# Optimization experiments

Hardware: AMD Instinct MI355X
Metric: run time of the kernel (lower is better)

Reference implementation:

```python
import jax, jax.numpy as jnp
import numpy as np

N_NODES = 20000
N_EDGES = 320000
NUM_GRAPHS = 64
IN_DIM = 256


def setup_inputs() -> dict:
    key = jax.random.key(0)
    ks = jax.random.split(key, 12)
    x = jax.random.normal(ks[0], (N_NODES, IN_DIM), dtype=jnp.float32)
    edge_index = jax.random.randint(ks[1], (2, N_EDGES), 0, N_NODES, dtype=jnp.int64)
    batch = jnp.sort(jax.random.randint(ks[2], (N_NODES,), 0, NUM_GRAPHS, dtype=jnp.int64))
    def glorot(k, shape):
        lim = float(np.sqrt(6.0 / (shape[0] + shape[1])))
        return jax.random.uniform(k, shape, dtype=jnp.float32, minval=-lim, maxval=lim)
    W1 = glorot(ks[3], (IN_DIM, 256)); b1 = jnp.zeros((256,), jnp.float32)
    W2 = glorot(ks[4], (256, 128));   b2 = jnp.zeros((128,), jnp.float32)
    Wl1 = glorot(ks[5], (128, 64));   bl1 = jnp.zeros((64,), jnp.float32)
    Wl2 = glorot(ks[6], (64, 1));     bl2 = jnp.zeros((1,), jnp.float32)
    return {"x": x, "edge_index": edge_index, "batch": batch,
            "W1": W1, "b1": b1, "W2": W2, "b2": b2,
            "Wl1": Wl1, "bl1": bl1, "Wl2": Wl2, "bl2": bl2}


def gcn_conv(x, src, dst, W, b, n_nodes):
    # PyG GCNConv: add self-loops, symmetric normalization D^-1/2 (A+I) D^-1/2,
    # linear transform first, then gather-scale-scatter aggregation, then bias.
    loop = jnp.arange(n_nodes, dtype=src.dtype)
    s = jnp.concatenate([src, loop])
    d = jnp.concatenate([dst, loop])
    deg = jax.ops.segment_sum(jnp.ones_like(d, dtype=x.dtype), d, num_segments=n_nodes)
    dinv = jnp.where(deg > 0, jax.lax.rsqrt(deg), 0.0)
    norm = dinv[s] * dinv[d]                         # [E+N]
    h = x @ W                                        # [N, out]
    msg = h[s] * norm[:, None]                       # [E+N, out]
    out = jax.ops.segment_sum(msg, d, num_segments=n_nodes)
    return out + b


def global_mean_pool(x, batch, num_graphs):
    sums = jax.ops.segment_sum(x, batch, num_segments=num_graphs)
    cnts = jax.ops.segment_sum(jnp.ones((x.shape[0],), x.dtype), batch, num_segments=num_graphs)
    return sums / jnp.maximum(cnts, 1.0)[:, None]


def reference(x, edge_index, batch, W1, b1, W2, b2, Wl1, bl1, Wl2, bl2):
    n = x.shape[0]
    src, dst = edge_index[0], edge_index[1]
    h = jax.nn.relu(gcn_conv(x, src, dst, W1, b1, n))   # dropout = identity (eval)
    h = jax.nn.relu(gcn_conv(h, src, dst, W2, b2, n))
    g = global_mean_pool(h, batch, NUM_GRAPHS)          # [G, 128]
    g = jax.nn.relu(g @ Wl1 + bl1)
    return jax.nn.sigmoid(g @ Wl2 + bl2)                # [G, 1]
```

## Files before the change

### kernel.cpp

```cpp
#include <hip/hip_runtime.h>
#include <hip/hip_bf16.h>
#include <math.h>

typedef __attribute__((ext_vector_type(8))) short bf16x8;
typedef __attribute__((ext_vector_type(4))) float f32x4;
typedef __attribute__((ext_vector_type(2))) float f32x2;

__device__ __forceinline__ unsigned short f2bf(float f) {
    unsigned int u = __float_as_uint(f);
    unsigned int r = (u + 0x7FFFu + ((u >> 16) & 1u)) >> 16;
    return (unsigned short)r;
}
__device__ __forceinline__ unsigned int pk2bf(float lo, float hi) {
    unsigned int r;
    asm("v_cvt_pk_bf16_f32 %0, %1, %2" : "=v"(r) : "v"(lo), "v"(hi));
    return r;
}
__device__ __forceinline__ unsigned char f2fp8(float v) {
    int p = __builtin_amdgcn_cvt_pk_fp8_f32(v, v, 0, false);
    return (unsigned char)(p & 0xff);
}
__device__ __forceinline__ unsigned int pk4fp8(float a, float b, float c, float d) {
    int p = __builtin_amdgcn_cvt_pk_fp8_f32(a, b, 0, false);
    p = __builtin_amdgcn_cvt_pk_fp8_f32(c, d, p, true);
    return (unsigned int)p;
}
#if __has_builtin(__builtin_amdgcn_cvt_pk_f32_fp8)
__device__ __forceinline__ void fp8x8_add(uint2 u, float* a) {
    f32x2 p0 = __builtin_amdgcn_cvt_pk_f32_fp8((int)u.x, false);
    f32x2 p1 = __builtin_amdgcn_cvt_pk_f32_fp8((int)u.x, true);
    f32x2 p2 = __builtin_amdgcn_cvt_pk_f32_fp8((int)u.y, false);
    f32x2 p3 = __builtin_amdgcn_cvt_pk_f32_fp8((int)u.y, true);
    a[0] += p0.x; a[1] += p0.y; a[2] += p1.x; a[3] += p1.y;
    a[4] += p2.x; a[5] += p2.y; a[6] += p3.x; a[7] += p3.y;
}
__device__ __forceinline__ void fp8x4_add(unsigned int u, float* a) {
    f32x2 p0 = __builtin_amdgcn_cvt_pk_f32_fp8((int)u, false);
    f32x2 p1 = __builtin_amdgcn_cvt_pk_f32_fp8((int)u, true);
    a[0] += p0.x; a[1] += p0.y; a[2] += p1.x; a[3] += p1.y;
}
#else
__device__ __forceinline__ void fp8x8_add(uint2 u, float* a) {
    a[0] += __builtin_amdgcn_cvt_f32_fp8((int)u.x, 0);
    a[1] += __builtin_amdgcn_cvt_f32_fp8((int)u.x, 1);
    a[2] += __builtin_amdgcn_cvt_f32_fp8((int)u.x, 2);
    a[3] += __builtin_amdgcn_cvt_f32_fp8((int)u.x, 3);
    a[4] += __builtin_amdgcn_cvt_f32_fp8((int)u.y, 0);
    a[5] += __builtin_amdgcn_cvt_f32_fp8((int)u.y, 1);
    a[6] += __builtin_amdgcn_cvt_f32_fp8((int)u.y, 2);
    a[7] += __builtin_amdgcn_cvt_f32_fp8((int)u.y, 3);
}
__device__ __forceinline__ void fp8x4_add(unsigned int u, float* a) {
    a[0] += __builtin_amdgcn_cvt_f32_fp8((int)u, 0);
    a[1] += __builtin_amdgcn_cvt_f32_fp8((int)u, 1);
    a[2] += __builtin_amdgcn_cvt_f32_fp8((int)u, 2);
    a[3] += __builtin_amdgcn_cvt_f32_fp8((int)u, 3);
}
#endif
__device__ __forceinline__ float deg_dinv(int c) { return rsqrtf((float)c + 1.0f); }

__device__ __forceinline__ void load_lds16(const unsigned short* g, unsigned short* l) {
    __builtin_amdgcn_global_load_lds(
        (const __attribute__((address_space(1))) unsigned int*)g,
        (__attribute__((address_space(3))) unsigned int*)l, 16, 0, 0);
}
__device__ __forceinline__ void load_lds16_u8(const unsigned char* g, unsigned char* l) {
    __builtin_amdgcn_global_load_lds(
        (const __attribute__((address_space(1))) unsigned int*)g,
        (__attribute__((address_space(3))) unsigned int*)l, 16, 0, 0);
}

__global__ __launch_bounds__(256) void prepfill_kernel(const int* __restrict__ src,
                                                       const int* __restrict__ dst,
                                                       int* __restrict__ cnt,
                                                       int* __restrict__ csr,
                                                       const int* __restrict__ batch,
                                                       int* __restrict__ gstart,
                                                       const float* __restrict__ W1,
                                                       unsigned short* __restrict__ w1t,
                                                       const float* __restrict__ W2,
                                                       unsigned char* __restrict__ w2t8,
                                                       int N, int G, int E, int FB, int CWB) {
    int b = blockIdx.x;
    int tid = threadIdx.x;
    if (b < FB) {
        int e = (b * 256 + tid) * 4;
        if (e + 3 < E) {
            int4 d4 = *(const int4*)(dst + e);
            int4 s4 = *(const int4*)(src + e);
            int sl;
            sl = atomicAdd(&cnt[d4.x], 1); if (sl < 64) csr[(d4.x << 6) + sl] = s4.x;
            sl = atomicAdd(&cnt[d4.y], 1); if (sl < 64) csr[(d4.y << 6) + sl] = s4.y;
            sl = atomicAdd(&cnt[d4.z], 1); if (sl < 64) csr[(d4.z << 6) + sl] = s4.z;
            sl = atomicAdd(&cnt[d4.w], 1); if (sl < 64) csr[(d4.w << 6) + sl] = s4.w;
        } else {
            for (; e < E; e++) {
                int d = dst[e];
                int slot = atomicAdd(&cnt[d], 1);
                if (slot < 64) csr[(d << 6) + slot] = src[e];
            }
        }
        return;
    }
    b -= FB;
    if (b < CWB) {
        int idx = b * 256 + tid;
        if (idx < 256 * 256) {
            int m = idx >> 8, k = idx & 255;
            w1t[idx] = f2bf(W1[(size_t)k * 256 + m]);
        } else if (idx < 256 * 256 + 128 * 256) {
            int j = idx - 256 * 256;
            int m = j >> 8, k = j & 255;
            w2t8[j] = f2fp8(W2[(size_t)k * 128 + m]);
        }
        return;
    }
    b -= CWB;
    {
        int i = b * 256 + tid;
        if (i >= N) return;
        int bb = batch[i];
        if (i == 0) { for (int g = 0; g <= bb; g++) gstart[g] = 0; }
        else { int bp = batch[i - 1]; for (int g = bp + 1; g <= bb; g++) gstart[g] = i; }
        if (i == N - 1) { for (int g = bb + 1; g <= G; g++) gstart[g] = N; }
    }
}

__global__ __launch_bounds__(256) void gemm1_kernel(const float* __restrict__ x,
                                                    const unsigned short* __restrict__ Bt,
                                                    const int* __restrict__ cnt,
                                                    unsigned char* __restrict__ C8, int N) {
    __shared__ unsigned short As[128 * 32];
    __shared__ unsigned short Bs[128 * 32];
    int gb = blockIdx.x;
    int bx = gb & 1, by = gb >> 1;
    const int K = 256;
    int tid = threadIdx.x;
    int wave = tid >> 6, lane = tid & 63;
    int quad = lane >> 4, m16 = lane & 15;
    int r0 = by * 128, c0 = bx * 128;
    int srow = lane >> 2;
    int skoff = (lane & 3) * 8;

    f32x4 acc[2][8];
#pragma unroll
    for (int rg = 0; rg < 2; rg++)
#pragma unroll
        for (int ct = 0; ct < 8; ct++) acc[rg][ct] = (f32x4){0.f, 0.f, 0.f, 0.f};

    int arow = tid >> 1, akh = tid & 1;
    int agrow = r0 + arow; if (agrow >= N) agrow = N - 1;
    const float* ap = x + (size_t)agrow * K + akh * 16;
    int asw = (arow >> 1) & 3;
    unsigned short* as0 = As + arow * 32 + ((((akh << 1) | 0) ^ asw) << 3);
    unsigned short* as1 = As + arow * 32 + ((((akh << 1) | 1) ^ asw) << 3);
    int rsw = (m16 >> 1) & 3;

    for (int kb = 0; kb < K; kb += 32) {
        float4 f0 = *(const float4*)(ap + kb);
        float4 f1 = *(const float4*)(ap + kb + 4);
        float4 f2 = *(const float4*)(ap + kb + 8);
        float4 f3 = *(const float4*)(ap + kb + 12);
        {
            int bcol = wave * 16 + srow;
            load_lds16(Bt + (size_t)(c0 + bcol) * K + kb + skoff, Bs + (wave * 16) * 32);
            load_lds16(Bt + (size_t)(c0 + 64 + bcol) * K + kb + skoff, Bs + (64 + wave * 16) * 32);
        }
        uint4 u0, u1;
        u0.x = pk2bf(f0.x, f0.y); u0.y = pk2bf(f0.z, f0.w);
        u0.z = pk2bf(f1.x, f1.y); u0.w = pk2bf(f1.z, f1.w);
        u1.x = pk2bf(f2.x, f2.y); u1.y = pk2bf(f2.z, f2.w);
        u1.z = pk2bf(f3.x, f3.y); u1.w = pk2bf(f3.z, f3.w);
        *(uint4*)as0 = u0;
        *(uint4*)as1 = u1;
        __syncthreads();
        bf16x8 af[2], bfr[8];
#pragma unroll
        for (int rg = 0; rg < 2; rg++)
            af[rg] = *(const bf16x8*)(As + (wave * 32 + rg * 16 + m16) * 32 + ((quad ^ rsw) << 3));
#pragma unroll
        for (int ct = 0; ct < 8; ct++)
            bfr[ct] = *(const bf16x8*)(Bs + (ct * 16 + m16) * 32 + (quad << 3));
#pragma unroll
        for (int rg = 0; rg < 2; rg++)
#pragma unroll
            for (int ct = 0; ct < 8; ct++)
                acc[rg][ct] = __builtin_amdgcn_mfma_f32_16x16x32_bf16(af[rg], bfr[ct], acc[rg][ct], 0, 0, 0);
        __syncthreads();
    }
    float di[2][4];
#pragma unroll
    for (int rg = 0; rg < 2; rg++)
#pragma unroll
        for (int r = 0; r < 4; r++) {
            int row = r0 + wave * 32 + rg * 16 + quad * 4 + r;
            di[rg][r] = (row < N) ? deg_dinv(cnt[row]) : 1.f;
        }
#pragma unroll
    for (int rg = 0; rg < 2; rg++) {
#pragma unroll
        for (int ct = 0; ct < 8; ct++) {
            int col = c0 + ct * 16 + m16;
#pragma unroll
            for (int r = 0; r < 4; r++) {
                int row = r0 + wave * 32 + rg * 16 + quad * 4 + r;
                if (row < N) C8[(size_t)row * 256 + col] = f2fp8(acc[rg][ct][r] * di[rg][r]);
            }
        }
    }
}

__global__ __launch_bounds__(256) void gemm2_kernel(const unsigned char* __restrict__ A,
                                                    const unsigned char* __restrict__ Bt,
                                                    const int* __restrict__ cnt,
                                                    unsigned char* __restrict__ C8, int N) {
    __shared__ unsigned char As8[128 * 32];
    __shared__ unsigned char Bs8[64 * 32];
    const int K = 256;
    int tid = threadIdx.x;
    int wave = tid >> 6, lane = tid & 63;
    int quad = lane >> 4, m16 = lane & 15;
    int bx = blockIdx.x, by = blockIdx.y;
    int r0 = by * 128, c0 = bx * 64;

    f32x4 acc[2][4];
#pragma unroll
    for (int rg = 0; rg < 2; rg++)
#pragma unroll
        for (int ct = 0; ct < 4; ct++) acc[rg][ct] = (f32x4){0.f, 0.f, 0.f, 0.f};

    int arow = wave * 32 + (lane >> 1);
    int agrow = r0 + arow; if (agrow >= N) agrow = N - 1;
    int ach = (lane & 1) * 16;
    int brow = (wave & 1) * 32 + (lane >> 1);
    int bch = (lane & 1) * 16;

    for (int kb = 0; kb < K; kb += 32) {
        load_lds16_u8(A + (size_t)agrow * K + kb + ach, As8 + (wave * 32) * 32);
        if (wave < 2)
            load_lds16_u8(Bt + (size_t)(c0 + brow) * K + kb + bch, Bs8 + (wave * 32) * 32);
        __syncthreads();
        long af[2], bfr[4];
#pragma unroll
        for (int rg = 0; rg < 2; rg++)
            af[rg] = *(const long*)(As8 + (wave * 32 + rg * 16 + m16) * 32 + (quad << 3));
#pragma unroll
        for (int ct = 0; ct < 4; ct++)
            bfr[ct] = *(const long*)(Bs8 + (ct * 16 + m16) * 32 + (quad << 3));
#pragma unroll
        for (int rg = 0; rg < 2; rg++)
#pragma unroll
            for (int ct = 0; ct < 4; ct++)
                acc[rg][ct] = __builtin_amdgcn_mfma_f32_16x16x32_fp8_fp8(af[rg], bfr[ct], acc[rg][ct], 0, 0, 0);
        __syncthreads();
    }
    float di[2][4];
#pragma unroll
    for (int rg = 0; rg < 2; rg++)
#pragma unroll
        for (int r = 0; r < 4; r++) {
            int row = r0 + wave * 32 + rg * 16 + quad * 4 + r;
            di[rg][r] = (row < N) ? deg_dinv(cnt[row]) : 1.f;
        }
#pragma unroll
    for (int rg = 0; rg < 2; rg++) {
#pragma unroll
        for (int ct = 0; ct < 4; ct++) {
            int col = c0 + ct * 16 + m16;
#pragma unroll
            for (int r = 0; r < 4; r++) {
                int row = r0 + wave * 32 + rg * 16 + quad * 4 + r;
                if (row < N) C8[(size_t)row * 128 + col] = f2fp8(acc[rg][ct][r] * di[rg][r]);
            }
        }
    }
}

__global__ __launch_bounds__(256) void gather256_kernel(const unsigned char* __restrict__ h8,
                                                        const int* __restrict__ csr,
                                                        const int* __restrict__ cnt,
                                                        const float* __restrict__ bias,
                                                        unsigned char* __restrict__ o18, int N) {
    int node = blockIdx.x * 4 + (threadIdx.x >> 6);
    if (node >= N) return;
    int lane = threadIdx.x & 63;
    int half = lane >> 5, hl = lane & 31;
    int beg = node << 6;
    int c = cnt[node];
    float dd = deg_dinv(c);
    if (c > 64) c = 64;
    int end = beg + c;
    uint2 uh = *(const uint2*)(h8 + (size_t)node * 256 + hl * 8);
    float a[8] = {0, 0, 0, 0, 0, 0, 0, 0};
    int j = beg;
    for (; j + 15 < end; j += 16) {
        int s0 = csr[j + half],      s1 = csr[j + 2 + half];
        int s2 = csr[j + 4 + half],  s3 = csr[j + 6 + half];
        int s4 = csr[j + 8 + half],  s5 = csr[j + 10 + half];
        int s6 = csr[j + 12 + half], s7 = csr[j + 14 + half];
        uint2 u0 = *(const uint2*)(h8 + (size_t)s0 * 256 + hl * 8);
        uint2 u1 = *(const uint2*)(h8 + (size_t)s1 * 256 + hl * 8);
        uint2 u2 = *(const uint2*)(h8 + (size_t)s2 * 256 + hl * 8);
        uint2 u3 = *(const uint2*)(h8 + (size_t)s3 * 256 + hl * 8);
        uint2 u4 = *(const uint2*)(h8 + (size_t)s4 * 256 + hl * 8);
        uint2 u5 = *(const uint2*)(h8 + (size_t)s5 * 256 + hl * 8);
        uint2 u6 = *(const uint2*)(h8 + (size_t)s6 * 256 + hl * 8);
        uint2 u7 = *(const uint2*)(h8 + (size_t)s7 * 256 + hl * 8);
        fp8x8_add(u0, a); fp8x8_add(u1, a); fp8x8_add(u2, a); fp8x8_add(u3, a);
        fp8x8_add(u4, a); fp8x8_add(u5, a); fp8x8_add(u6, a); fp8x8_add(u7, a);
    }
    for (; j + 7 < end; j += 8) {
        int s0 = csr[j + half], s1 = csr[j + 2 + half];
        int s2 = csr[j + 4 + half], s3 = csr[j + 6 + half];
        uint2 u0 = *(const uint2*)(h8 + (size_t)s0 * 256 + hl * 8);
        uint2 u1 = *(const uint2*)(h8 + (size_t)s1 * 256 + hl * 8);
        uint2 u2 = *(const uint2*)(h8 + (size_t)s2 * 256 + hl * 8);
        uint2 u3 = *(const uint2*)(h8 + (size_t)s3 * 256 + hl * 8);
        fp8x8_add(u0, a); fp8x8_add(u1, a); fp8x8_add(u2, a); fp8x8_add(u3, a);
    }
    for (; j + 1 < end; j += 2) {
        int s0 = csr[j + half];
        uint2 u0 = *(const uint2*)(h8 + (size_t)s0 * 256 + hl * 8);
        fp8x8_add(u0, a);
    }
    if (j < end && half == 0) {
        int s0 = csr[j];
        uint2 u0 = *(const uint2*)(h8 + (size_t)s0 * 256 + hl * 8);
        fp8x8_add(u0, a);
    }
#pragma unroll
    for (int i = 0; i < 8; i++) a[i] += __shfl_down(a[i], 32);
    if (half == 0) {
        float self[8] = {0, 0, 0, 0, 0, 0, 0, 0};
        fp8x8_add(uh, self);
        float4 bv0 = ((const float4*)bias)[hl * 2];
        float4 bv1 = ((const float4*)bias)[hl * 2 + 1];
        float bvf[8] = {bv0.x, bv0.y, bv0.z, bv0.w, bv1.x, bv1.y, bv1.z, bv1.w};
        float v[8];
#pragma unroll
        for (int i = 0; i < 8; i++) v[i] = fmaxf((a[i] + self[i]) * dd + bvf[i], 0.f);
        uint2 o;
        o.x = pk4fp8(v[0], v[1], v[2], v[3]);
        o.y = pk4fp8(v[4], v[5], v[6], v[7]);
        ((uint2*)(o18 + (size_t)node * 256))[hl] = o;
    }
}

__global__ __launch_bounds__(256) void gather128_kernel(const unsigned char* __restrict__ t8,
                                                        const int* __restrict__ csr,
                                                        const int* __restrict__ cnt,
                                                        const float* __restrict__ bias,
                                                        unsigned char* __restrict__ out2, int N) {
    int node = blockIdx.x * 4 + (threadIdx.x >> 6);
    if (node >= N) return;
    int lane = threadIdx.x & 63;
    int half = lane >> 5, hl = lane & 31;
    int beg = node << 6;
    int c = cnt[node];
    float dd = deg_dinv(c);
    if (c > 64) c = 64;
    int end = beg + c;
    unsigned int uh = *(const unsigned int*)(t8 + (size_t)node * 128 + hl * 4);
    float a[4] = {0, 0, 0, 0};
    int j = beg;
    for (; j + 15 < end; j += 16) {
        int s0 = csr[j + half],      s1 = csr[j + 2 + half];
        int s2 = csr[j + 4 + half],  s3 = csr[j + 6 + half];
        int s4 = csr[j + 8 + half],  s5 = csr[j + 10 + half];
        int s6 = csr[j + 12 + half], s7 = csr[j + 14 + half];
        unsigned int u0 = *(const unsigned int*)(t8 + (size_t)s0 * 128 + hl * 4);
        unsigned int u1 = *(const unsigned int*)(t8 + (size_t)s1 * 128 + hl * 4);
        unsigned int u2 = *(const unsigned int*)(t8 + (size_t)s2 * 128 + hl * 4);
        unsigned int u3 = *(const unsigned int*)(t8 + (size_t)s3 * 128 + hl * 4);
        unsigned int u4 = *(const unsigned int*)(t8 + (size_t)s4 * 128 + hl * 4);
        unsigned int u5 = *(const unsigned int*)(t8 + (size_t)s5 * 128 + hl * 4);
        unsigned int u6 = *(const unsigned int*)(t8 + (size_t)s6 * 128 + hl * 4);
        unsigned int u7 = *(const unsigned int*)(t8 + (size_t)s7 * 128 + hl * 4);
        fp8x4_add(u0, a); fp8x4_add(u1, a); fp8x4_add(u2, a); fp8x4_add(u3, a);
        fp8x4_add(u4, a); fp8x4_add(u5, a); fp8x4_add(u6, a); fp8x4_add(u7, a);
    }
    for (; j + 7 < end; j += 8) {
        int s0 = csr[j + half], s1 = csr[j + 2 + half];
        int s2 = csr[j + 4 + half], s3 = csr[j + 6 + half];
        unsigned int u0 = *(const unsigned int*)(t8 + (size_t)s0 * 128 + hl * 4);
        unsigned int u1 = *(const unsigned int*)(t8 + (size_t)s1 * 128 + hl * 4);
        unsigned int u2 = *(const unsigned int*)(t8 + (size_t)s2 * 128 + hl * 4);
        unsigned int u3 = *(const unsigned int*)(t8 + (size_t)s3 * 128 + hl * 4);
        fp8x4_add(u0, a); fp8x4_add(u1, a); fp8x4_add(u2, a); fp8x4_add(u3, a);
    }
    for (; j + 1 < end; j += 2) {
        int s0 = csr[j + half];
        unsigned int u0 = *(const unsigned int*)(t8 + (size_t)s0 * 128 + hl * 4);
        fp8x4_add(u0, a);
    }
    if (j < end && half == 0) {
        int s0 = csr[j];
        unsigned int u0 = *(const unsigned int*)(t8 + (size_t)s0 * 128 + hl * 4);
        fp8x4_add(u0, a);
    }
#pragma unroll
    for (int i = 0; i < 4; i++) a[i] += __shfl_down(a[i], 32);
    if (half == 0) {
        float self[4] = {0, 0, 0, 0};
        fp8x4_add(uh, self);
        float4 bv = ((const float4*)bias)[hl];
        float r0 = fmaxf((a[0] + self[0]) * dd + bv.x, 0.f);
        float r1 = fmaxf((a[1] + self[1]) * dd + bv.y, 0.f);
        float r2 = fmaxf((a[2] + self[2]) * dd + bv.z, 0.f);
        float r3 = fmaxf((a[3] + self[3]) * dd + bv.w, 0.f);
        ((unsigned int*)(out2 + (size_t)node * 128))[hl] = pk4fp8(r0, r1, r2, r3);
    }
}

__global__ __launch_bounds__(256) void poolhead_kernel(const unsigned char* __restrict__ out2,
                                                       const int* __restrict__ gstart,
                                                       float* __restrict__ gsum,
                                                       int* __restrict__ gdone,
                                                       const float* __restrict__ Wl1,
                                                       const float* __restrict__ bl1,
                                                       const float* __restrict__ Wl2,
                                                       const float* __restrict__ bl2,
                                                       float* __restrict__ out) {
    int g = blockIdx.x >> 3, slice = blockIdx.x & 7;
    int tid = threadIdx.x;
    int hw = tid >> 5, hl = tid & 31;
    int gs = gstart[g], ge = gstart[g + 1];
    float a[4] = {0, 0, 0, 0};
    for (int i = gs + slice * 8 + hw; i < ge; i += 64) {
        unsigned int u = ((const unsigned int*)(out2 + (size_t)i * 128))[hl];
        fp8x4_add(u, a);
    }
    __shared__ float red[8][128];
#pragma unroll
    for (int k = 0; k < 4; k++) red[hw][hl * 4 + k] = a[k];
    __syncthreads();
    if (tid < 128) {
        float s = 0.f;
#pragma unroll
        for (int w = 0; w < 8; w++) s += red[w][tid];
        if (s != 0.f) atomicAdd(&gsum[g * 128 + tid], s);
    }
    __syncthreads();
    __shared__ int lastflag;
    if (tid == 0) {
        __threadfence();
        int old = atomicAdd(&gdone[g], 1);
        lastflag = (old == 7) ? 1 : 0;
    }
    __syncthreads();
    if (!lastflag) return;
    __shared__ float gv[128];
    if (tid < 128) {
        float s = atomicAdd(&gsum[g * 128 + tid], 0.0f);
        float cntf = fmaxf((float)(ge - gs), 1.0f);
        gv[tid] = s / cntf;
    }
    __syncthreads();
    if (tid < 64) {
        float acc = bl1[tid];
#pragma unroll 8
        for (int k = 0; k < 128; k++) acc += gv[k] * Wl1[k * 64 + tid];
        acc = fmaxf(acc, 0.f);
        float p = acc * Wl2[tid];
#pragma unroll
        for (int off = 32; off; off >>= 1) p += __shfl_down(p, off);
        if (tid == 0) out[g] = 1.f / (1.f + expf(-(p + bl2[0])));
    }
}

extern "C" void kernel_launch(void* const* d_in, const int* in_sizes, int n_in,
                              void* d_out, int out_size, void* d_ws, size_t ws_size,
                              hipStream_t stream) {
    const float* x   = (const float*)d_in[0];
    const int* ei    = (const int*)d_in[1];
    const int* batch = (const int*)d_in[2];
    const float* W1  = (const float*)d_in[3];
    const float* b1  = (const float*)d_in[4];
    const float* W2  = (const float*)d_in[5];
    const float* b2  = (const float*)d_in[6];
    const float* Wl1 = (const float*)d_in[7];
    const float* bl1 = (const float*)d_in[8];
    const float* Wl2 = (const float*)d_in[9];
    const float* bl2 = (const float*)d_in[10];
    float* out = (float*)d_out;

    const int N = in_sizes[2];
    const int E = in_sizes[1] / 2;
    const int G = 64;
    const int* src = ei;
    const int* dst = ei + E;

    char* base = (char*)d_ws;
    size_t off = 0;
    auto carve = [&](size_t bytes) -> char* {
        char* p = base + off;
        off = (off + bytes + 15) & ~(size_t)15;
        return p;
    };
    int*   cnt    = (int*)carve((size_t)N * 4);
    float* gsum   = (float*)carve((size_t)G * 128 * 4);
    int*   gdone  = (int*)carve((size_t)G * 4);
    size_t zero_bytes = (size_t)(N + G * 128 + G) * 4 + 32;
    int*   csr    = (int*)carve((size_t)N * 64 * 4);
    int*   gstart = (int*)carve((size_t)(G + 1) * 4);
    unsigned short* w1t  = (unsigned short*)carve((size_t)256 * 256 * 2);
    unsigned char*  w2t8 = (unsigned char*)carve((size_t)128 * 256);
    unsigned char*  h8   = (unsigned char*)carve((size_t)N * 256);
    unsigned char*  o18  = (unsigned char*)carve((size_t)N * 256);
    unsigned char*  t8   = h8;
    unsigned char*  out2 = o18;

    hipMemsetAsync(d_ws, 0, zero_bytes, stream);

    const int BNB = (N + 255) / 256;
    const int CWB = (256 * 256 + 128 * 256 + 255) / 256;
    const int FB  = (E / 4 + 255) / 256;
    prepfill_kernel<<<FB + CWB + BNB, 256, 0, stream>>>(src, dst, cnt, csr, batch, gstart,
                                                        W1, w1t, W2, w2t8, N, G, E, FB, CWB);

    const int GB1 = 2 * ((N + 127) / 128);
    gemm1_kernel<<<GB1, 256, 0, stream>>>(x, w1t, cnt, h8, N);

    gather256_kernel<<<(N + 3) / 4, 256, 0, stream>>>(h8, csr, cnt, b1, o18, N);

    {
        dim3 grid(2, (N + 127) / 128);
        gemm2_kernel<<<grid, 256, 0, stream>>>(o18, w2t8, cnt, t8, N);
    }
    gather128_kernel<<<(N + 3) / 4, 256, 0, stream>>>(t8, csr, cnt, b2, out2, N);

    poolhead_kernel<<<G * 8, 256, 0, stream>>>(out2, gstart, gsum, gdone,
                                               Wl1, bl1, Wl2, bl2, out);
}
```

Baseline: 173.1 us.

## Fuse layer-1 neighbor aggregation into GEMM2 via LDS-resident tiles

```diff
diff --git a/kernel.cpp b/kernel.cpp
--- a/kernel.cpp
+++ b/kernel.cpp
@@ -210,139 +210,128 @@
     }
 }
 
-__global__ __launch_bounds__(256) void gemm2_kernel(const unsigned char* __restrict__ A,
-                                                    const unsigned char* __restrict__ Bt,
-                                                    const int* __restrict__ cnt,
-                                                    unsigned char* __restrict__ C8, int N) {
-    __shared__ unsigned char As8[128 * 32];
-    __shared__ unsigned char Bs8[64 * 32];
-    const int K = 256;
+__global__ __launch_bounds__(512) void l1agg_gemm2_kernel(const unsigned char* __restrict__ h8,
+                                                          const int* __restrict__ csr,
+                                                          const int* __restrict__ cnt,
+                                                          const float* __restrict__ b1,
+                                                          const unsigned char* __restrict__ w2t8,
+                                                          unsigned char* __restrict__ t8,
+                                                          int N) {
+    __shared__ unsigned char As8[64 * 256];
+    __shared__ unsigned char Bs8[128 * 256];
     int tid = threadIdx.x;
     int wave = tid >> 6, lane = tid & 63;
+    int r0 = blockIdx.x * 64;
+
+#pragma unroll
+    for (int q = 0; q < 4; q++) {
+        int s = q * 512 + wave * 64 + lane;
+        int r = s >> 4, sr = s & 15;
+        int gs = sr ^ (r & 7);
+        load_lds16_u8(w2t8 + (size_t)r * 256 + gs * 16,
+                      Bs8 + ((size_t)q * 512 + wave * 64) * 16);
+    }
+
+    int half_id = tid >> 5, hl = tid & 31;
+    float4 bv0 = ((const float4*)b1)[hl * 2];
+    float4 bv1 = ((const float4*)b1)[hl * 2 + 1];
+    float bvf[8] = {bv0.x, bv0.y, bv0.z, bv0.w, bv1.x, bv1.y, bv1.z, bv1.w};
+#pragma unroll
+    for (int t = 0; t < 4; t++) {
+        int nl = t * 16 + half_id;
+        int n = r0 + nl;
+        if (n < N) {
+            int c = cnt[n];
+            float dd = deg_dinv(c);
+            if (c > 64) c = 64;
+            int beg = n << 6, end = beg + c;
+            uint2 uh = *(const uint2*)(h8 + (size_t)n * 256 + hl * 8);
+            float a[8] = {0, 0, 0, 0, 0, 0, 0, 0};
+            int j = beg;
+            for (; j + 7 < end; j += 8) {
+                int s0 = csr[j + 0], s1 = csr[j + 1], s2 = csr[j + 2], s3 = csr[j + 3];
+                int s4 = csr[j + 4], s5 = csr[j + 5], s6 = csr[j + 6], s7 = csr[j + 7];
+                uint2 u0 = *(const uint2*)(h8 + (size_t)s0 * 256 + hl * 8);
+                uint2 u1 = *(const uint2*)(h8 + (size_t)s1 * 256 + hl * 8);
+                uint2 u2 = *(const uint2*)(h8 + (size_t)s2 * 256 + hl * 8);
+                uint2 u3 = *(const uint2*)(h8 + (size_t)s3 * 256 + hl * 8);
+                uint2 u4 = *(const uint2*)(h8 + (size_t)s4 * 256 + hl * 8);
+                uint2 u5 = *(const uint2*)(h8 + (size_t)s5 * 256 + hl * 8);
+                uint2 u6 = *(const uint2*)(h8 + (size_t)s6 * 256 + hl * 8);
+                uint2 u7 = *(const uint2*)(h8 + (size_t)s7 * 256 + hl * 8);
+                fp8x8_add(u0, a); fp8x8_add(u1, a); fp8x8_add(u2, a); fp8x8_add(u3, a);
+                fp8x8_add(u4, a); fp8x8_add(u5, a); fp8x8_add(u6, a); fp8x8_add(u7, a);
+            }
+            for (; j + 3 < end; j += 4) {
+                int s0 = csr[j + 0], s1 = csr[j + 1], s2 = csr[j + 2], s3 = csr[j + 3];
+                uint2 u0 = *(const uint2*)(h8 + (size_t)s0 * 256 + hl * 8);
+                uint2 u1 = *(const uint2*)(h8 + (size_t)s1 * 256 + hl * 8);
+                uint2 u2 = *(const uint2*)(h8 + (size_t)s2 * 256 + hl * 8);
+                uint2 u3 = *(const uint2*)(h8 + (size_t)s3 * 256 + hl * 8);
+                fp8x8_add(u0, a); fp8x8_add(u1, a); fp8x8_add(u2, a); fp8x8_add(u3, a);
+            }
+            for (; j < end; j++) {
+                int s0 = csr[j];
+                uint2 u0 = *(const uint2*)(h8 + (size_t)s0 * 256 + hl * 8);
+                fp8x8_add(u0, a);
+            }
+            float self[8] = {0, 0, 0, 0, 0, 0, 0, 0};
+            fp8x8_add(uh, self);
+            float v[8];
+#pragma unroll
+            for (int i = 0; i < 8; i++) v[i] = fmaxf((a[i] + self[i]) * dd + bvf[i], 0.f);
+            uint2 o;
+            o.x = pk4fp8(v[0], v[1], v[2], v[3]);
+            o.y = pk4fp8(v[4], v[5], v[6], v[7]);
+            *(uint2*)(As8 + nl * 256 + ((hl * 8) ^ ((nl & 7) << 4))) = o;
+        }
+    }
+    __syncthreads();
+
     int quad = lane >> 4, m16 = lane & 15;
-    int bx = blockIdx.x, by = blockIdx.y;
-    int r0 = by * 128, c0 = bx * 64;
-
-    f32x4 acc[2][4];
-#pragma unroll
-    for (int rg = 0; rg < 2; rg++)
-#pragma unroll
-        for (int ct = 0; ct < 4; ct++) acc[rg][ct] = (f32x4){0.f, 0.f, 0.f, 0.f};
-
-    int arow = wave * 32 + (lane >> 1);
-    int agrow = r0 + arow; if (agrow >= N) agrow = N - 1;
-    int ach = (lane & 1) * 16;
-    int brow = (wave & 1) * 32 + (lane >> 1);
-    int bch = (lane & 1) * 16;
-
-    for (int kb = 0; kb < K; kb += 32) {
-        load_lds16_u8(A + (size_t)agrow * K + kb + ach, As8 + (wave * 32) * 32);
-        if (wave < 2)
-            load_lds16_u8(Bt + (size_t)(c0 + brow) * K + kb + bch, Bs8 + (wave * 32) * 32);
-        __syncthreads();
-        long af[2], bfr[4];
-#pragma unroll
-        for (int rg = 0; rg < 2; rg++)
-            af[rg] = *(const long*)(As8 + (wave * 32 + rg * 16 + m16) * 32 + (quad << 3));
-#pragma unroll
-        for (int ct = 0; ct < 4; ct++)
-            bfr[ct] = *(const long*)(Bs8 + (ct * 16 + m16) * 32 + (quad << 3));
-#pragma unroll
-        for (int rg = 0; rg < 2; rg++)
-#pragma unroll
-            for (int ct = 0; ct < 4; ct++)
-                acc[rg][ct] = __builtin_amdgcn_mfma_f32_16x16x32_fp8_fp8(af[rg], bfr[ct], acc[rg][ct], 0, 0, 0);
-        __syncthreads();
-    }
-    float di[2][4];
-#pragma unroll
-    for (int rg = 0; rg < 2; rg++)
+    int wr = wave >> 2, wc = wave & 3;
+    f32x4 acc[2][2];
+#pragma unroll
+    for (int rf = 0; rf < 2; rf++)
+#pragma unroll
+        for (int cf = 0; cf < 2; cf++) acc[rf][cf] = (f32x4){0.f, 0.f, 0.f, 0.f};
+#pragma unroll
+    for (int kb = 0; kb < 8; kb++) {
+        int byt = kb * 32 + quad * 8;
+        long af[2], bfr[2];
+#pragma unroll
+        for (int rf = 0; rf < 2; rf++) {
+            int row = wr * 32 + rf * 16 + m16;
+            af[rf] = *(const long*)(As8 + row * 256 + (byt ^ ((row & 7) << 4)));
+        }
+#pragma unroll
+        for (int cf = 0; cf < 2; cf++) {
+            int col = wc * 32 + cf * 16 + m16;
+            bfr[cf] = *(const long*)(Bs8 + col * 256 + (byt ^ ((col & 7) << 4)));
+        }
+#pragma unroll
+        for (int rf = 0; rf < 2; rf++)
+#pragma unroll
+            for (int cf = 0; cf < 2; cf++)
+                acc[rf][cf] = __builtin_amdgcn_mfma_f32_16x16x32_fp8_fp8(af[rf], bfr[cf], acc[rf][cf], 0, 0, 0);
+    }
+#pragma unroll
+    for (int rf = 0; rf < 2; rf++) {
+        float di[4];
 #pragma unroll
         for (int r = 0; r < 4; r++) {
-            int row = r0 + wave * 32 + rg * 16 + quad * 4 + r;
-            di[rg][r] = (row < N) ? deg_dinv(cnt[row]) : 1.f;
-        }
-#pragma unroll
-    for (int rg = 0; rg < 2; rg++) {
-#pragma unroll
-        for (int ct = 0; ct < 4; ct++) {
-            int col = c0 + ct * 16 + m16;
+            int row = r0 + wr * 32 + rf * 16 + quad * 4 + r;
+            di[r] = (row < N) ? deg_dinv(cnt[row]) : 1.f;
+        }
+#pragma unroll
+        for (int cf = 0; cf < 2; cf++) {
+            int col = wc * 32 + cf * 16 + m16;
 #pragma unroll
             for (int r = 0; r < 4; r++) {
-                int row = r0 + wave * 32 + rg * 16 + quad * 4 + r;
-                if (row < N) C8[(size_t)row * 128 + col] = f2fp8(acc[rg][ct][r] * di[rg][r]);
+                int row = r0 + wr * 32 + rf * 16 + quad * 4 + r;
+                if (row < N) t8[(size_t)row * 128 + col] = f2fp8(acc[rf][cf][r] * di[r]);
             }
         }
-    }
-}
-
-__global__ __launch_bounds__(256) void gather256_kernel(const unsigned char* __restrict__ h8,
-                                                        const int* __restrict__ csr,
-                                                        const int* __restrict__ cnt,
-                                                        const float* __restrict__ bias,
-                                                        unsigned char* __restrict__ o18, int N) {
-    int node = blockIdx.x * 4 + (threadIdx.x >> 6);
-    if (node >= N) return;
-    int lane = threadIdx.x & 63;
-    int half = lane >> 5, hl = lane & 31;
-    int beg = node << 6;
-    int c = cnt[node];
-    float dd = deg_dinv(c);
-    if (c > 64) c = 64;
-    int end = beg + c;
-    uint2 uh = *(const uint2*)(h8 + (size_t)node * 256 + hl * 8);
-    float a[8] = {0, 0, 0, 0, 0, 0, 0, 0};
-    int j = beg;
-    for (; j + 15 < end; j += 16) {
-        int s0 = csr[j + half],      s1 = csr[j + 2 + half];
-        int s2 = csr[j + 4 + half],  s3 = csr[j + 6 + half];
-        int s4 = csr[j + 8 + half],  s5 = csr[j + 10 + half];
-        int s6 = csr[j + 12 + half], s7 = csr[j + 14 + half];
-        uint2 u0 = *(const uint2*)(h8 + (size_t)s0 * 256 + hl * 8);
-        uint2 u1 = *(const uint2*)(h8 + (size_t)s1 * 256 + hl * 8);
-        uint2 u2 = *(const uint2*)(h8 + (size_t)s2 * 256 + hl * 8);
-        uint2 u3 = *(const uint2*)(h8 + (size_t)s3 * 256 + hl * 8);
-        uint2 u4 = *(const uint2*)(h8 + (size_t)s4 * 256 + hl * 8);
-        uint2 u5 = *(const uint2*)(h8 + (size_t)s5 * 256 + hl * 8);
-        uint2 u6 = *(const uint2*)(h8 + (size_t)s6 * 256 + hl * 8);
-        uint2 u7 = *(const uint2*)(h8 + (size_t)s7 * 256 + hl * 8);
-        fp8x8_add(u0, a); fp8x8_add(u1, a); fp8x8_add(u2, a); fp8x8_add(u3, a);
-        fp8x8_add(u4, a); fp8x8_add(u5, a); fp8x8_add(u6, a); fp8x8_add(u7, a);
-    }
-    for (; j + 7 < end; j += 8) {
-        int s0 = csr[j + half], s1 = csr[j + 2 + half];
-        int s2 = csr[j + 4 + half], s3 = csr[j + 6 + half];
-        uint2 u0 = *(const uint2*)(h8 + (size_t)s0 * 256 + hl * 8);
-        uint2 u1 = *(const uint2*)(h8 + (size_t)s1 * 256 + hl * 8);
-        uint2 u2 = *(const uint2*)(h8 + (size_t)s2 * 256 + hl * 8);
-        uint2 u3 = *(const uint2*)(h8 + (size_t)s3 * 256 + hl * 8);
-        fp8x8_add(u0, a); fp8x8_add(u1, a); fp8x8_add(u2, a); fp8x8_add(u3, a);
-    }
-    for (; j + 1 < end; j += 2) {
-        int s0 = csr[j + half];
-        uint2 u0 = *(const uint2*)(h8 + (size_t)s0 * 256 + hl * 8);
-        fp8x8_add(u0, a);
-    }
-    if (j < end && half == 0) {
-        int s0 = csr[j];
-        uint2 u0 = *(const uint2*)(h8 + (size_t)s0 * 256 + hl * 8);
-        fp8x8_add(u0, a);
-    }
-#pragma unroll
-    for (int i = 0; i < 8; i++) a[i] += __shfl_down(a[i], 32);
-    if (half == 0) {
-        float self[8] = {0, 0, 0, 0, 0, 0, 0, 0};
-        fp8x8_add(uh, self);
-        float4 bv0 = ((const float4*)bias)[hl * 2];
-        float4 bv1 = ((const float4*)bias)[hl * 2 + 1];
-        float bvf[8] = {bv0.x, bv0.y, bv0.z, bv0.w, bv1.x, bv1.y, bv1.z, bv1.w};
-        float v[8];
-#pragma unroll
-        for (int i = 0; i < 8; i++) v[i] = fmaxf((a[i] + self[i]) * dd + bvf[i], 0.f);
-        uint2 o;
-        o.x = pk4fp8(v[0], v[1], v[2], v[3]);
-        o.y = pk4fp8(v[4], v[5], v[6], v[7]);
-        ((uint2*)(o18 + (size_t)node * 256))[hl] = o;
     }
 }
 
@@ -506,9 +495,8 @@
     unsigned short* w1t  = (unsigned short*)carve((size_t)256 * 256 * 2);
     unsigned char*  w2t8 = (unsigned char*)carve((size_t)128 * 256);
     unsigned char*  h8   = (unsigned char*)carve((size_t)N * 256);
-    unsigned char*  o18  = (unsigned char*)carve((size_t)N * 256);
-    unsigned char*  t8   = h8;
-    unsigned char*  out2 = o18;
+    unsigned char*  t8   = (unsigned char*)carve((size_t)N * 128);
+    unsigned char*  out2 = (unsigned char*)carve((size_t)N * 128);
 
     hipMemsetAsync(d_ws, 0, zero_bytes, stream);
 
@@ -521,12 +509,8 @@
     const int GB1 = 2 * ((N + 127) / 128);
     gemm1_kernel<<<GB1, 256, 0, stream>>>(x, w1t, cnt, h8, N);
 
-    gather256_kernel<<<(N + 3) / 4, 256, 0, stream>>>(h8, csr, cnt, b1, o18, N);
-
-    {
-        dim3 grid(2, (N + 127) / 128);
-        gemm2_kernel<<<grid, 256, 0, stream>>>(o18, w2t8, cnt, t8, N);
-    }
+    l1agg_gemm2_kernel<<<(N + 63) / 64, 512, 0, stream>>>(h8, csr, cnt, b1, w2t8, t8, N);
+
     gather128_kernel<<<(N + 3) / 4, 256, 0, stream>>>(t8, csr, cnt, b2, out2, N);
 
     poolhead_kernel<<<G * 8, 256, 0, stream>>>(out2, gstart, gsum, gdone,
```

Measured after the change: 174.4 us. No clear change (+0.7%).
